# Kernel tuning notes

Measured on AMD Instinct MI355X. Metric: run time of the kernel, lower is better.

Reference implementation:

```python
import jax, jax.numpy as jnp
import numpy as np

N_HEADS = 4
N_HIDDEN = 512  # out_features with concat=False
SLOPE = 0.01
NEG = -1e9


def setup_inputs() -> dict:
    key = jax.random.key(0)
    k1, k2, k3, k4 = jax.random.split(key, 4)
    N, F_IN = 8192, 512
    h = jax.random.normal(k1, (N, F_IN), dtype=jnp.float32)
    W = jax.random.normal(k2, (F_IN, N_HIDDEN * N_HEADS), dtype=jnp.float32) * 0.05
    a = jax.random.normal(k3, (N_HEADS, 2 * N_HIDDEN, 1), dtype=jnp.float32) * 0.05
    adj_mat = jnp.where(jax.random.uniform(k4, (N, N)) < 0.01, 0.0, NEG).astype(jnp.float32)
    return {"h": h, "adj_mat": adj_mat, "W": W, "a": a}


def reference(h, adj_mat, W, a):
    N = h.shape[0]
    # [N, H*d] -> [H, N, d]
    ht = (h @ W).reshape(N, N_HEADS, N_HIDDEN).transpose(1, 0, 2)
    a_src = a[:, :N_HIDDEN, 0]   # [H, d]
    a_dst = a[:, N_HIDDEN:, 0]   # [H, d]
    src = jnp.einsum('hnd,hd->hn', ht, a_src)  # [H, N]
    dst = jnp.einsum('hnd,hd->hn', ht, a_dst)  # [H, N]
    # e[h,i,j] = leaky_relu(src[h,i] + dst[h,j]) + adj_mat[i,j]
    e = jax.nn.leaky_relu(src[:, :, None] + dst[:, None, :], SLOPE) + adj_mat[None]
    att = jax.nn.softmax(e, axis=-1)           # [H, N, N]
    h_prime = jnp.einsum('hij,hjd->hid', att, ht)  # [H, N, d]
    return h_prime.mean(axis=0)                # concat=False -> head mean, [N, d]
```

## Files before the change

### kernel.cpp

```cpp
#include <hip/hip_runtime.h>
#include <stdint.h>

#define NN 8192
#define DH 512
#define NH 4
#define LOG2E 1.4426950408889634f

typedef __attribute__((ext_vector_type(8))) short short8;
typedef __attribute__((ext_vector_type(4))) float f32x4;

__device__ __forceinline__ unsigned short f2bf(float f) {
    unsigned int u = __float_as_uint(f);
    unsigned int r = (u + 0x7fffu + ((u >> 16) & 1u)) >> 16;
    return (unsigned short)r;
}
__device__ __forceinline__ float bf2f(unsigned short s) {
    return __uint_as_float(((unsigned int)s) << 16);
}

__device__ __forceinline__ void global_to_lds16(const void* g, void* l) {
    __builtin_amdgcn_global_load_lds(
        (const __attribute__((address_space(1))) unsigned int*)g,
        (__attribute__((address_space(3))) unsigned int*)l, 16, 0, 0);
}

__global__ void k_convert_h(const float* __restrict__ hf, unsigned short* __restrict__ hb) {
    const int idx = (blockIdx.x * 256 + threadIdx.x) * 8;
    const float4 f0 = *(const float4*)(hf + idx);
    const float4 f1 = *(const float4*)(hf + idx + 4);
    uint4 o;
    o.x = (unsigned)f2bf(f0.x) | ((unsigned)f2bf(f0.y) << 16);
    o.y = (unsigned)f2bf(f0.z) | ((unsigned)f2bf(f0.w) << 16);
    o.z = (unsigned)f2bf(f1.x) | ((unsigned)f2bf(f1.y) << 16);
    o.w = (unsigned)f2bf(f1.z) | ((unsigned)f2bf(f1.w) << 16);
    *(uint4*)(hb + idx) = o;
}

__global__ void k_transpose_W(const float* __restrict__ W, unsigned short* __restrict__ Wt) {
    __shared__ float t[32][33];
    const int tx = threadIdx.x & 31, ty = threadIdx.x >> 5;
    const int p0 = blockIdx.x * 32, k0 = blockIdx.y * 32;
#pragma unroll
    for (int r = 0; r < 4; r++)
        t[ty + r * 8][tx] = W[(k0 + ty + r * 8) * 2048 + p0 + tx];
    __syncthreads();
#pragma unroll
    for (int r = 0; r < 4; r++)
        Wt[(size_t)(p0 + ty + r * 8) * 512 + k0 + tx] = f2bf(t[tx][ty + r * 8]);
}

__global__ __launch_bounds__(256, 3) void k_gemm(const unsigned short* __restrict__ Wt,
                                                 const unsigned short* __restrict__ hb,
                                                 unsigned short* __restrict__ vt) {
    __shared__ alignas(16) char smem[32768];
    const int tid = threadIdx.x;
    const int w = tid >> 6, lane = tid & 63;
    const int lr = lane & 15, lc = lane >> 4;
    const int pBase = blockIdx.y * 128, nBase = blockIdx.x * 128;
    f32x4 acc[4][4] = {};
    const int wr = (w >> 1) * 64, wc = (w & 1) * 64;
    for (int kb = 0; kb < 8; kb++) {
        const int k0 = kb * 64;
#pragma unroll
        for (int it = 0; it < 4; it++) {
            const int o = it * 4096 + w * 1024 + lane * 16;
            const int row = o >> 7;
            const int koff = (o & 127) >> 1;
            global_to_lds16(Wt + (size_t)(pBase + row) * 512 + k0 + koff,
                            smem + it * 4096 + w * 1024);
            global_to_lds16(hb + (size_t)(nBase + row) * 512 + k0 + koff,
                            smem + 16384 + it * 4096 + w * 1024);
        }
        __syncthreads();
#pragma unroll
        for (int kk = 0; kk < 2; kk++) {
            short8 a[4], b[4];
#pragma unroll
            for (int m = 0; m < 4; m++)
                a[m] = *(const short8*)(smem + (wr + m * 16 + lr) * 128 + kk * 64 + lc * 16);
#pragma unroll
            for (int n = 0; n < 4; n++)
                b[n] = *(const short8*)(smem + 16384 + (wc + n * 16 + lr) * 128 + kk * 64 + lc * 16);
#pragma unroll
            for (int m = 0; m < 4; m++)
#pragma unroll
                for (int n = 0; n < 4; n++)
                    acc[m][n] = __builtin_amdgcn_mfma_f32_16x16x32_bf16(a[m], b[n], acc[m][n], 0, 0, 0);
        }
        __syncthreads();
    }
#pragma unroll
    for (int m = 0; m < 4; m++)
#pragma unroll
        for (int n = 0; n < 4; n++)
#pragma unroll
            for (int q = 0; q < 4; q++) {
                const int p = pBase + wr + m * 16 + lc * 4 + q;
                const int ncol = nBase + wc + n * 16 + lr;
                vt[(size_t)p * NN + ncol] = f2bf(acc[m][n][q]);
            }
}

__global__ void k_srcdst(const unsigned short* __restrict__ vt, const float* __restrict__ a,
                         float* __restrict__ srcL, float* __restrict__ dstL) {
    const int n = blockIdx.x * 256 + threadIdx.x;
    const int h = blockIdx.y;
    const int d0 = blockIdx.z * 64;
    float s = 0.f, t = 0.f;
#pragma unroll 4
    for (int d = d0; d < d0 + 64; d++) {
        const float v = bf2f(vt[(size_t)(h * 512 + d) * NN + n]);
        s += v * a[h * 1024 + d];
        t += v * a[h * 1024 + 512 + d];
    }
    __hip_atomic_fetch_add(&srcL[h * NN + n], s * LOG2E, __ATOMIC_RELAXED, __HIP_MEMORY_SCOPE_AGENT);
    __hip_atomic_fetch_add(&dstL[h * NN + n], t * LOG2E, __ATOMIC_RELAXED, __HIP_MEMORY_SCOPE_AGENT);
}

#define D_OFF 114688
#define NJT (NN / 32)
__global__ __launch_bounds__(512, 2) void k_flash(const float* __restrict__ adj,
                                                  const unsigned short* __restrict__ vt,
                                                  const float* __restrict__ srcL,
                                                  const float* __restrict__ dstL,
                                                  float* __restrict__ out) {
    __shared__ alignas(16) char smem[115200];
    const int tid = threadIdx.x;
    const int w = tid >> 6, lane = tid & 63;
    const int lr = lane & 15, lc = lane >> 4;
    const int h = blockIdx.x & 3;
    const int i0 = (int)(blockIdx.x >> 2) * 128;
    const int ih = w >> 2, dq = w & 3;
    float* denom = (float*)(smem + D_OFF);

    const int srow = i0 + w * 16 + lr;
    const float srcv = srcL[h * NN + srow];
    const float* __restrict__ adjp = adj + (size_t)srow * NN + lc * 8;
    const float* __restrict__ dlp = dstL + h * NN + lc * 8;
    const unsigned short* __restrict__ vth = vt + (size_t)(h * 512) * NN;
    float dsum = 0.f;
    f32x4 acc[4][8] = {};

    unsigned voff[4];
#pragma unroll
    for (int it = 0; it < 4; it++) {
        const int o = it * 8192 + w * 1024 + lane * 16;
        const int row = o >> 7;
        const int z = ((o >> 4) & 7) ^ (row & 7);
        const int d = (row << 1) | (z >> 2);
        voff[it] = (unsigned)d * NN + ((z & 3) << 3);
    }
    const int prow = w * 16 + lr;
    const int psl = (((prow & 1) << 2) | lc) ^ ((prow >> 1) & 7);
    const int poff = (prow >> 1) * 128 + (psl << 4);

    char* vc = smem;
    char* vn = smem + 32768;
    char* vnn = smem + 65536;
    char* pc = smem + 98304;
    char* pn = smem + 106496;

#define STAGE(J0, DST)                                                                   \
    {                                                                                    \
        _Pragma("unroll") for (int it = 0; it < 4; it++)                                 \
            global_to_lds16(vth + voff[it] + (J0), (DST) + it * 8192 + w * 1024);        \
    }

#define LOADROW(J0)                                                                      \
    {                                                                                    \
        aj0 = *(const float4*)(adjp + (J0));                                             \
        aj1 = *(const float4*)(adjp + (J0) + 4);                                         \
        dl0 = *(const float4*)(dlp + (J0));                                              \
        dl1 = *(const float4*)(dlp + (J0) + 4);                                          \
    }

#define SCORE()                                                                          \
    {                                                                                    \
        const float padj[8] = {aj0.x, aj0.y, aj0.z, aj0.w, aj1.x, aj1.y, aj1.z, aj1.w};  \
        const float pdst[8] = {dl0.x, dl0.y, dl0.z, dl0.w, dl1.x, dl1.y, dl1.z, dl1.w};  \
        _Pragma("unroll") for (int q = 0; q < 8; q++) {                                  \
            const float x = srcv + pdst[q];                                              \
            const float l2 = fmaxf(x, 0.01f * x);                                        \
            const float p = exp2f(l2 + padj[q]);                                         \
            dsum += p;                                                                   \
            pfrag[q] = (short)f2bf(p);                                                   \
        }                                                                                \
    }

#define PV(VBUF, PBUF)                                                                   \
    {                                                                                    \
        const char* vb = (VBUF);                                                         \
        const char* pb = (PBUF);                                                         \
        short8 afr[4];                                                                   \
        _Pragma("unroll") for (int t = 0; t < 4; t++) {                                  \
            const int rr = ih * 64 + t * 16 + lr;                                        \
            const int sl = (((rr & 1) << 2) | lc) ^ ((rr >> 1) & 7);                     \
            afr[t] = *(const short8*)(pb + (rr >> 1) * 128 + (sl << 4));                 \
        }                                                                                \
        __builtin_amdgcn_s_setprio(1);                                                   \
        _Pragma("unroll") for (int s = 0; s < 8; s++) {                                  \
            const int d = dq * 128 + s * 16 + lr;                                        \
            const int sl = (((d & 1) << 2) | lc) ^ ((d >> 1) & 7);                       \
            const short8 bfr = *(const short8*)(vb + (d >> 1) * 128 + (sl << 4));        \
            _Pragma("unroll") for (int t = 0; t < 4; t++)                                \
                acc[t][s] = __builtin_amdgcn_mfma_f32_16x16x32_bf16(afr[t], bfr,         \
                                                                    acc[t][s], 0, 0, 0); \
        }                                                                                \
        __builtin_amdgcn_s_setprio(0);                                                   \
    }

    float4 aj0, aj1, dl0, dl1;
    short8 pfrag;
    LOADROW(0);
    STAGE(0, vc);
    SCORE();
    *(short8*)(pc + poff) = pfrag;
#pragma unroll 1
    for (int jb = 0; jb < NJT - 1; jb++) {
        const int J0 = (jb + 1) * 32;
        LOADROW(J0);
        STAGE(J0, vn);
        asm volatile("s_waitcnt vmcnt(8) lgkmcnt(0)" ::: "memory");
        __builtin_amdgcn_sched_barrier(0);
        __builtin_amdgcn_s_barrier();
        __builtin_amdgcn_sched_barrier(0);
        PV(vc, pc);
        SCORE();
        *(short8*)(pn + poff) = pfrag;
        char* tv = vc; vc = vn; vn = vnn; vnn = tv;
        char* tp = pc; pc = pn; pn = tp;
    }
    asm volatile("s_waitcnt vmcnt(0) lgkmcnt(0)" ::: "memory");
    __builtin_amdgcn_sched_barrier(0);
    __builtin_amdgcn_s_barrier();
    __builtin_amdgcn_sched_barrier(0);
    PV(vc, pc);

    dsum += __shfl_xor(dsum, 16, 64);
    dsum += __shfl_xor(dsum, 32, 64);
    if (lane < 16) denom[w * 16 + lane] = dsum;
    __syncthreads();
#pragma unroll
    for (int t = 0; t < 4; t++) {
        const int rl = ih * 64 + t * 16 + lc * 4;
#pragma unroll
        for (int q = 0; q < 4; q++) {
            const float inv = 0.25f / denom[rl + q];
            float* orow = out + (size_t)(i0 + rl + q) * 512;
#pragma unroll
            for (int s = 0; s < 8; s++) {
                const int d = dq * 128 + s * 16 + lr;
                __hip_atomic_fetch_add(orow + d, acc[t][s][q] * inv,
                                       __ATOMIC_RELAXED, __HIP_MEMORY_SCOPE_AGENT);
            }
        }
    }
}

extern "C" void kernel_launch(void* const* d_in, const int* in_sizes, int n_in,
                              void* d_out, int out_size, void* d_ws, size_t ws_size,
                              hipStream_t stream) {
    const float* h = (const float*)d_in[0];
    const float* adj = (const float*)d_in[1];
    const float* W = (const float*)d_in[2];
    const float* a = (const float*)d_in[3];
    float* out = (float*)d_out;
    char* ws = (char*)d_ws;
    unsigned short* hb = (unsigned short*)ws;
    unsigned short* Wt = (unsigned short*)(ws + 8388608);
    unsigned short* vt = (unsigned short*)(ws + 8388608 + 2097152);
    float* srcL = (float*)(ws + 8388608 + 2097152 + 33554432);
    float* dstL = srcL + NH * NN;

    hipMemsetAsync(d_out, 0, (size_t)out_size * sizeof(float), stream);
    hipMemsetAsync(srcL, 0, 2 * NH * NN * sizeof(float), stream);
    k_convert_h<<<2048, 256, 0, stream>>>(h, hb);
    k_transpose_W<<<dim3(64, 16), 256, 0, stream>>>(W, Wt);
    k_gemm<<<dim3(64, 16), 256, 0, stream>>>(Wt, hb, vt);
    k_srcdst<<<dim3(32, NH, 8), 256, 0, stream>>>(vt, a, srcL, dstL);
    k_flash<<<256, 512, 0, stream>>>(adj, vt, srcL, dstL, out);
}
```

Measured before the change: 808.8 us.

## Fuse src/dst projection into GEMM epilogue and deepen flash-attention prefetch pipeline

The separate k_srcdst kernel is removed. The attention-logit projections are now computed from fp32 GEMM accumulators in the k_gemm epilogue, using wave shuffles and atomics, which avoids re-reading the bf16 vt buffer and one launch. In k_flash the V staging goes from a 3-buffer to a 4-buffer ring with two tiles in flight and double-buffered adjacency/dst registers, and the loop is unrolled by four with fixed buffer pointers. exp2 and bf16 packing use inline v_exp_f32 and v_cvt_pk_bf16_f32. LDS grows to about 148KB, which limits occupancy to one block per CU, and src/dst are now computed from unrounded fp32 values.

```diff
diff --git a/kernel.cpp b/kernel.cpp
--- a/kernel.cpp
+++ b/kernel.cpp
@@ -13,9 +13,6 @@
     unsigned int u = __float_as_uint(f);
     unsigned int r = (u + 0x7fffu + ((u >> 16) & 1u)) >> 16;
     return (unsigned short)r;
-}
-__device__ __forceinline__ float bf2f(unsigned short s) {
-    return __uint_as_float(((unsigned int)s) << 16);
 }
 
 __device__ __forceinline__ void global_to_lds16(const void* g, void* l) {
@@ -51,7 +48,10 @@
 
 __global__ __launch_bounds__(256, 3) void k_gemm(const unsigned short* __restrict__ Wt,
                                                  const unsigned short* __restrict__ hb,
-                                                 unsigned short* __restrict__ vt) {
+                                                 unsigned short* __restrict__ vt,
+                                                 const float* __restrict__ a,
+                                                 float* __restrict__ srcL,
+                                                 float* __restrict__ dstL) {
     __shared__ alignas(16) char smem[32768];
     const int tid = threadIdx.x;
     const int w = tid >> 6, lane = tid & 63;
@@ -74,18 +74,18 @@
         __syncthreads();
 #pragma unroll
         for (int kk = 0; kk < 2; kk++) {
-            short8 a[4], b[4];
+            short8 av[4], bv[4];
 #pragma unroll
             for (int m = 0; m < 4; m++)
-                a[m] = *(const short8*)(smem + (wr + m * 16 + lr) * 128 + kk * 64 + lc * 16);
+                av[m] = *(const short8*)(smem + (wr + m * 16 + lr) * 128 + kk * 64 + lc * 16);
 #pragma unroll
             for (int n = 0; n < 4; n++)
-                b[n] = *(const short8*)(smem + 16384 + (wc + n * 16 + lr) * 128 + kk * 64 + lc * 16);
+                bv[n] = *(const short8*)(smem + 16384 + (wc + n * 16 + lr) * 128 + kk * 64 + lc * 16);
 #pragma unroll
             for (int m = 0; m < 4; m++)
 #pragma unroll
                 for (int n = 0; n < 4; n++)
-                    acc[m][n] = __builtin_amdgcn_mfma_f32_16x16x32_bf16(a[m], b[n], acc[m][n], 0, 0, 0);
+                    acc[m][n] = __builtin_amdgcn_mfma_f32_16x16x32_bf16(av[m], bv[n], acc[m][n], 0, 0, 0);
         }
         __syncthreads();
     }
@@ -99,39 +99,63 @@
                 const int ncol = nBase + wc + n * 16 + lr;
                 vt[(size_t)p * NN + ncol] = f2bf(acc[m][n][q]);
             }
-}
-
-__global__ void k_srcdst(const unsigned short* __restrict__ vt, const float* __restrict__ a,
-                         float* __restrict__ srcL, float* __restrict__ dstL) {
-    const int n = blockIdx.x * 256 + threadIdx.x;
-    const int h = blockIdx.y;
-    const int d0 = blockIdx.z * 64;
-    float s = 0.f, t = 0.f;
-#pragma unroll 4
-    for (int d = d0; d < d0 + 64; d++) {
-        const float v = bf2f(vt[(size_t)(h * 512 + d) * NN + n]);
-        s += v * a[h * 1024 + d];
-        t += v * a[h * 1024 + 512 + d];
-    }
-    __hip_atomic_fetch_add(&srcL[h * NN + n], s * LOG2E, __ATOMIC_RELAXED, __HIP_MEMORY_SCOPE_AGENT);
-    __hip_atomic_fetch_add(&dstL[h * NN + n], t * LOG2E, __ATOMIC_RELAXED, __HIP_MEMORY_SCOPE_AGENT);
-}
-
-#define D_OFF 114688
+    const int hh = pBase >> 9;
+    const float* __restrict__ ah = a + hh * 1024;
+    float ssum[4] = {0.f, 0.f, 0.f, 0.f}, tsum[4] = {0.f, 0.f, 0.f, 0.f};
+#pragma unroll
+    for (int m = 0; m < 4; m++) {
+        const int dbase = (pBase & 511) + wr + m * 16 + lc * 4;
+#pragma unroll
+        for (int q = 0; q < 4; q++) {
+            const float as = ah[dbase + q];
+            const float ad = ah[512 + dbase + q];
+#pragma unroll
+            for (int n = 0; n < 4; n++) {
+                ssum[n] += acc[m][n][q] * as;
+                tsum[n] += acc[m][n][q] * ad;
+            }
+        }
+    }
+#pragma unroll
+    for (int n = 0; n < 4; n++) {
+        ssum[n] += __shfl_xor(ssum[n], 16, 64);
+        ssum[n] += __shfl_xor(ssum[n], 32, 64);
+        tsum[n] += __shfl_xor(tsum[n], 16, 64);
+        tsum[n] += __shfl_xor(tsum[n], 32, 64);
+    }
+    if (lane < 16) {
+#pragma unroll
+        for (int n = 0; n < 4; n++) {
+            const int ncol = nBase + wc + n * 16 + lane;
+            __hip_atomic_fetch_add(&srcL[hh * NN + ncol], ssum[n] * LOG2E,
+                                   __ATOMIC_RELAXED, __HIP_MEMORY_SCOPE_AGENT);
+            __hip_atomic_fetch_add(&dstL[hh * NN + ncol], tsum[n] * LOG2E,
+                                   __ATOMIC_RELAXED, __HIP_MEMORY_SCOPE_AGENT);
+        }
+    }
+}
+
 #define NJT (NN / 32)
 __global__ __launch_bounds__(512, 2) void k_flash(const float* __restrict__ adj,
                                                   const unsigned short* __restrict__ vt,
                                                   const float* __restrict__ srcL,
                                                   const float* __restrict__ dstL,
                                                   float* __restrict__ out) {
-    __shared__ alignas(16) char smem[115200];
+    __shared__ alignas(16) char smem[147968];
+    char* const vb0 = smem;
+    char* const vb1 = smem + 32768;
+    char* const vb2 = smem + 65536;
+    char* const vb3 = smem + 98304;
+    char* const p0lds = smem + 131072;
+    char* const p1lds = smem + 139264;
+    float* denom = (float*)(smem + 147456);
+
     const int tid = threadIdx.x;
     const int w = tid >> 6, lane = tid & 63;
     const int lr = lane & 15, lc = lane >> 4;
     const int h = blockIdx.x & 3;
     const int i0 = (int)(blockIdx.x >> 2) * 128;
     const int ih = w >> 2, dq = w & 3;
-    float* denom = (float*)(smem + D_OFF);
 
     const int srow = i0 + w * 16 + lr;
     const float srcv = srcL[h * NN + srow];
@@ -154,54 +178,63 @@
     const int psl = (((prow & 1) << 2) | lc) ^ ((prow >> 1) & 7);
     const int poff = (prow >> 1) * 128 + (psl << 4);
 
-    char* vc = smem;
-    char* vn = smem + 32768;
-    char* vnn = smem + 65536;
-    char* pc = smem + 98304;
-    char* pn = smem + 106496;
-
 #define STAGE(J0, DST)                                                                   \
     {                                                                                    \
         _Pragma("unroll") for (int it = 0; it < 4; it++)                                 \
             global_to_lds16(vth + voff[it] + (J0), (DST) + it * 8192 + w * 1024);        \
     }
 
-#define LOADROW(J0)                                                                      \
+#define LOADROW_A(J0)                                                                    \
+    ajA0 = *(const float4*)(adjp + (J0));                                                \
+    ajA1 = *(const float4*)(adjp + (J0) + 4);                                            \
+    dlA0 = *(const float4*)(dlp + (J0));                                                 \
+    dlA1 = *(const float4*)(dlp + (J0) + 4);
+
+#define LOADROW_B(J0)                                                                    \
+    ajB0 = *(const float4*)(adjp + (J0));                                                \
+    ajB1 = *(const float4*)(adjp + (J0) + 4);                                            \
+    dlB0 = *(const float4*)(dlp + (J0));                                                 \
+    dlB1 = *(const float4*)(dlp + (J0) + 4);
+
+#define SCORE_IMPL(AJ0, AJ1, DL0, DL1)                                                   \
     {                                                                                    \
-        aj0 = *(const float4*)(adjp + (J0));                                             \
-        aj1 = *(const float4*)(adjp + (J0) + 4);                                         \
-        dl0 = *(const float4*)(dlp + (J0));                                              \
-        dl1 = *(const float4*)(dlp + (J0) + 4);                                          \
-    }
-
-#define SCORE()                                                                          \
-    {                                                                                    \
-        const float padj[8] = {aj0.x, aj0.y, aj0.z, aj0.w, aj1.x, aj1.y, aj1.z, aj1.w};  \
-        const float pdst[8] = {dl0.x, dl0.y, dl0.z, dl0.w, dl1.x, dl1.y, dl1.z, dl1.w};  \
+        const float padj[8] = {AJ0.x, AJ0.y, AJ0.z, AJ0.w, AJ1.x, AJ1.y, AJ1.z, AJ1.w}; \
+        const float pdst[8] = {DL0.x, DL0.y, DL0.z, DL0.w, DL1.x, DL1.y, DL1.z, DL1.w}; \
+        float pv[8];                                                                     \
         _Pragma("unroll") for (int q = 0; q < 8; q++) {                                  \
             const float x = srcv + pdst[q];                                              \
             const float l2 = fmaxf(x, 0.01f * x);                                        \
-            const float p = exp2f(l2 + padj[q]);                                         \
-            dsum += p;                                                                   \
-            pfrag[q] = (short)f2bf(p);                                                   \
+            float e;                                                                     \
+            asm("v_exp_f32 %0, %1" : "=v"(e) : "v"(l2 + padj[q]));                       \
+            dsum += e;                                                                   \
+            pv[q] = e;                                                                   \
         }                                                                                \
-    }
+        union { unsigned u[4]; short8 s; } pk;                                           \
+        asm("v_cvt_pk_bf16_f32 %0, %1, %2" : "=v"(pk.u[0]) : "v"(pv[0]), "v"(pv[1]));    \
+        asm("v_cvt_pk_bf16_f32 %0, %1, %2" : "=v"(pk.u[1]) : "v"(pv[2]), "v"(pv[3]));    \
+        asm("v_cvt_pk_bf16_f32 %0, %1, %2" : "=v"(pk.u[2]) : "v"(pv[4]), "v"(pv[5]));    \
+        asm("v_cvt_pk_bf16_f32 %0, %1, %2" : "=v"(pk.u[3]) : "v"(pv[6]), "v"(pv[7]));    \
+        pfrag = pk.s;                                                                    \
+    }
+
+#define SCORE_A() SCORE_IMPL(ajA0, ajA1, dlA0, dlA1)
+#define SCORE_B() SCORE_IMPL(ajB0, ajB1, dlB0, dlB1)
 
 #define PV(VBUF, PBUF)                                                                   \
     {                                                                                    \
-        const char* vb = (VBUF);                                                         \
-        const char* pb = (PBUF);                                                         \
+        const char* vbp = (VBUF);                                                        \
+        const char* pbp = (PBUF);                                                        \
         short8 afr[4];                                                                   \
         _Pragma("unroll") for (int t = 0; t < 4; t++) {                                  \
             const int rr = ih * 64 + t * 16 + lr;                                        \
             const int sl = (((rr & 1) << 2) | lc) ^ ((rr >> 1) & 7);                     \
-            afr[t] = *(const short8*)(pb + (rr >> 1) * 128 + (sl << 4));                 \
+            afr[t] = *(const short8*)(pbp + (rr >> 1) * 128 + (sl << 4));                \
         }                                                                                \
         __builtin_amdgcn_s_setprio(1);                                                   \
         _Pragma("unroll") for (int s = 0; s < 8; s++) {                                  \
             const int d = dq * 128 + s * 16 + lr;                                        \
             const int sl = (((d & 1) << 2) | lc) ^ ((d >> 1) & 7);                       \
-            const short8 bfr = *(const short8*)(vb + (d >> 1) * 128 + (sl << 4));        \
+            const short8 bfr = *(const short8*)(vbp + (d >> 1) * 128 + (sl << 4));       \
             _Pragma("unroll") for (int t = 0; t < 4; t++)                                \
                 acc[t][s] = __builtin_amdgcn_mfma_f32_16x16x32_bf16(afr[t], bfr,         \
                                                                     acc[t][s], 0, 0, 0); \
@@ -209,32 +242,66 @@
         __builtin_amdgcn_s_setprio(0);                                                   \
     }
 
-    float4 aj0, aj1, dl0, dl1;
+#define WAITBAR(N)                                                                       \
+    asm volatile("s_waitcnt vmcnt(" #N ") lgkmcnt(0)" ::: "memory");                     \
+    __builtin_amdgcn_sched_barrier(0);                                                   \
+    __builtin_amdgcn_s_barrier();                                                        \
+    __builtin_amdgcn_sched_barrier(0);
+
+#define BODY0(JB)                       \
+    LOADROW_A(((JB) + 2) * 32);         \
+    STAGE(((JB) + 2) * 32, vb2);        \
+    WAITBAR(16);                        \
+    PV(vb0, p0lds);                     \
+    SCORE_B();                          \
+    *(short8*)(p1lds + poff) = pfrag;
+#define BODY1(JB)                       \
+    LOADROW_B(((JB) + 2) * 32);         \
+    STAGE(((JB) + 2) * 32, vb3);        \
+    WAITBAR(16);                        \
+    PV(vb1, p1lds);                     \
+    SCORE_A();                          \
+    *(short8*)(p0lds + poff) = pfrag;
+#define BODY2(JB)                       \
+    LOADROW_A(((JB) + 2) * 32);         \
+    STAGE(((JB) + 2) * 32, vb0);        \
+    WAITBAR(16);                        \
+    PV(vb2, p0lds);                     \
+    SCORE_B();                          \
+    *(short8*)(p1lds + poff) = pfrag;
+#define BODY3(JB)                       \
+    LOADROW_B(((JB) + 2) * 32);         \
+    STAGE(((JB) + 2) * 32, vb1);        \
+    WAITBAR(16);                        \
+    PV(vb3, p1lds);                     \
+    SCORE_A();                          \
+    *(short8*)(p0lds + poff) = pfrag;
+
+    float4 ajA0, ajA1, dlA0, dlA1;
+    float4 ajB0, ajB1, dlB0, dlB1;
     short8 pfrag;
-    LOADROW(0);
-    STAGE(0, vc);
-    SCORE();
-    *(short8*)(pc + poff) = pfrag;
+    LOADROW_A(0);
+    STAGE(0, vb0);
+    LOADROW_B(32);
+    STAGE(32, vb1);
+    SCORE_A();
+    *(short8*)(p0lds + poff) = pfrag;
+    WAITBAR(8);
 #pragma unroll 1
-    for (int jb = 0; jb < NJT - 1; jb++) {
-        const int J0 = (jb + 1) * 32;
-        LOADROW(J0);
-        STAGE(J0, vn);
-        asm volatile("s_waitcnt vmcnt(8) lgkmcnt(0)" ::: "memory");
-        __builtin_amdgcn_sched_barrier(0);
-        __builtin_amdgcn_s_barrier();
-        __builtin_amdgcn_sched_barrier(0);
-        PV(vc, pc);
-        SCORE();
-        *(short8*)(pn + poff) = pfrag;
-        char* tv = vc; vc = vn; vn = vnn; vnn = tv;
-        char* tp = pc; pc = pn; pn = tp;
-    }
-    asm volatile("s_waitcnt vmcnt(0) lgkmcnt(0)" ::: "memory");
-    __builtin_amdgcn_sched_barrier(0);
-    __builtin_amdgcn_s_barrier();
-    __builtin_amdgcn_sched_barrier(0);
-    PV(vc, pc);
+    for (int jb = 0; jb < NJT - 4; jb += 4) {
+        BODY0(jb + 0);
+        BODY1(jb + 1);
+        BODY2(jb + 2);
+        BODY3(jb + 3);
+    }
+    BODY0(NJT - 4);
+    BODY1(NJT - 3);
+    WAITBAR(8);
+    PV(vb2, p0lds);
+    SCORE_B();
+    *(short8*)(p1lds + poff) = pfrag;
+    WAITBAR(0);
+    PV(vb3, p1lds);
 
     dsum += __shfl_xor(dsum, 16, 64);
     dsum += __shfl_xor(dsum, 32, 64);
@@ -276,7 +343,6 @@
     hipMemsetAsync(srcL, 0, 2 * NH * NN * sizeof(float), stream);
     k_convert_h<<<2048, 256, 0, stream>>>(h, hb);
     k_transpose_W<<<dim3(64, 16), 256, 0, stream>>>(W, Wt);
-    k_gemm<<<dim3(64, 16), 256, 0, stream>>>(Wt, hb, vt);
-    k_srcdst<<<dim3(32, NH, 8), 256, 0, stream>>>(vt, a, srcL, dstL);
+    k_gemm<<<dim3(64, 16), 256, 0, stream>>>(Wt, hb, vt, a, srcL, dstL);
     k_flash<<<256, 512, 0, stream>>>(adj, vt, srcL, dstL, out);
 }
```

Result: slower. 1.105 ms (+36.7%).
